# Optimization experiments

Hardware: AMD Instinct MI355X
Metric: run time of the kernel (lower is better)

Reference implementation:

```python
import jax, jax.numpy as jnp
import numpy as np

EPS = 1e-5
HEADS = 4


def _ln(x, s, b):
    m = jnp.mean(x, axis=-1, keepdims=True)
    v = jnp.mean(jnp.square(x - m), axis=-1, keepdims=True)
    return (x - m) * jax.lax.rsqrt(v + EPS) * s + b


def _gru(x, Wg, bg, Wcx, bcx, Wch, bch):
    # In this GRUCell the gates depend only on the inputs, so the gate and
    # candidate_x matmuls are precomputed over all timesteps; only the
    # (reset*h) @ Wch matmul is sequential.
    gx = jax.nn.sigmoid(x @ Wg + bg)   # [B,S,2H]
    cx = x @ Wcx + bcx                 # [B,S,H]
    H = Wch.shape[0]

    def step(h, gc):
        g, c = gc
        r, u = jnp.split(g, 2, axis=-1)
        cand = jnp.tanh(c + (r * h) @ Wch + bch)
        h_new = u * h + (1.0 - u) * cand
        return h_new, h_new

    h0 = jnp.zeros((x.shape[0], H), x.dtype)
    _, ys = jax.lax.scan(step, h0, (gx.transpose(1, 0, 2), cx.transpose(1, 0, 2)))
    return ys.transpose(1, 0, 2)


def _attn(x, s, b, Wq, bq, Wk, bk, Wv, bv, Wo, bo):
    skip = x
    xn = _ln(x, s, b)
    B, S, _ = xn.shape
    QKV = Wq.shape[1]
    hd = QKV // HEADS
    q = (xn @ Wq + bq).reshape(B, S, HEADS, hd)
    k = (xn @ Wk + bk).reshape(B, S, HEADS, hd)
    v = (xn @ Wv + bv).reshape(B, S, HEADS, hd)
    scores = jnp.einsum('bqhd,bkhd->bhqk', q, k) / jnp.sqrt(jnp.asarray(hd, x.dtype))
    probs = jax.nn.softmax(scores, axis=-1)
    o = jnp.einsum('bhqk,bkhd->bqhd', probs, v).reshape(B, S, QKV)
    return o @ Wo + bo + skip


def _forward(x_cgm, x_other, W_in, b_in, ln0_s, ln0_b,
             g0_Wg, g0_bg, g0_Wcx, g0_bcx, g0_Wch, g0_bch, ln1_s, ln1_b,
             g1_Wg, g1_bg, g1_Wcx, g1_bcx, g1_Wch, g1_bch, ln2_s, ln2_b,
             aln_s, aln_b, Wq, bq, Wk, bk, Wv, bv, Wo, bo,
             Wd1, bd1, lnd1_s, lnd1_b, Wd2, bd2, lnd2_s, lnd2_b, Wout, bout):
    # input projection + LN
    x = _ln(x_cgm @ W_in + b_in, ln0_s, ln0_b)
    # GRU block 0 (residual: dims match, 256==256)
    y = _gru(x, g0_Wg, g0_bg, g0_Wcx, g0_bcx, g0_Wch, g0_bch)
    x = _ln(y, ln1_s, ln1_b) + x
    # GRU block 1
    y = _gru(x, g1_Wg, g1_bg, g1_Wcx, g1_bcx, g1_Wch, g1_bch)
    x = _ln(y, ln2_s, ln2_b) + x
    # attention block after every 2nd GRU block
    x = _attn(x, aln_s, aln_b, Wq, bq, Wk, bk, Wv, bv, Wo, bo)
    # pool over time, concat static features, dense head (no residuals: dims differ)
    pooled = jnp.mean(x, axis=1)
    c = jnp.concatenate([pooled, x_other], axis=-1)
    c = _ln(jax.nn.relu(c @ Wd1 + bd1), lnd1_s, lnd1_b)
    c = _ln(jax.nn.relu(c @ Wd2 + bd2), lnd2_s, lnd2_b)
    return (c @ Wout + bout).squeeze(-1)


def setup_inputs() -> dict:
    key = jax.random.key(0)
    ks = iter(jax.random.split(key, 64))

    def nrm(shape, scale=1.0):
        return jax.random.normal(next(ks), shape, jnp.float32) * scale

    B, S, Fc, Fo, D, QKV = 64, 288, 16, 32, 256, 64
    inp = {
        'x_cgm': nrm((B, S, Fc)),
        'x_other': nrm((B, Fo)),
        'W_in': nrm((Fc, D), Fc ** -0.5), 'b_in': jnp.zeros((D,), jnp.float32),
        'ln0_s': jnp.ones((D,), jnp.float32), 'ln0_b': jnp.zeros((D,), jnp.float32),
    }
    for p in ('g0', 'g1'):
        inp[p + '_Wg'] = nrm((D, 2 * D), D ** -0.5)
        inp[p + '_bg'] = jnp.zeros((2 * D,), jnp.float32)
        inp[p + '_Wcx'] = nrm((D, D), D ** -0.5)
        inp[p + '_bcx'] = jnp.zeros((D,), jnp.float32)
        inp[p + '_Wch'] = nrm((D, D), D ** -0.5)
        inp[p + '_bch'] = jnp.zeros((D,), jnp.float32)
    for n in ('ln1', 'ln2', 'aln'):
        inp[n + '_s'] = jnp.ones((D,), jnp.float32)
        inp[n + '_b'] = jnp.zeros((D,), jnp.float32)
    for n in ('Wq', 'Wk', 'Wv'):
        inp[n] = nrm((D, QKV), D ** -0.5)
    for n in ('bq', 'bk', 'bv'):
        inp[n] = jnp.zeros((QKV,), jnp.float32)
    inp['Wo'] = nrm((QKV, D), QKV ** -0.5)
    inp['bo'] = jnp.zeros((D,), jnp.float32)
    inp['Wd1'] = nrm((D + Fo, 128), (D + Fo) ** -0.5)
    inp['bd1'] = jnp.zeros((128,), jnp.float32)
    inp['lnd1_s'] = jnp.ones((128,), jnp.float32)
    inp['lnd1_b'] = jnp.zeros((128,), jnp.float32)
    inp['Wd2'] = nrm((128, 64), 128 ** -0.5)
    inp['bd2'] = jnp.zeros((64,), jnp.float32)
    inp['lnd2_s'] = jnp.ones((64,), jnp.float32)
    inp['lnd2_b'] = jnp.zeros((64,), jnp.float32)
    inp['Wout'] = nrm((64, 1), 64 ** -0.5)
    inp['bout'] = jnp.zeros((1,), jnp.float32)
    return inp


def reference(x_cgm, x_other, W_in, b_in, ln0_s, ln0_b,
              g0_Wg, g0_bg, g0_Wcx, g0_bcx, g0_Wch, g0_bch, ln1_s, ln1_b,
              g1_Wg, g1_bg, g1_Wcx, g1_bcx, g1_Wch, g1_bch, ln2_s, ln2_b,
              aln_s, aln_b, Wq, bq, Wk, bk, Wv, bv, Wo, bo,
              Wd1, bd1, lnd1_s, lnd1_b, Wd2, bd2, lnd2_s, lnd2_b, Wout, bout):
    return _forward(x_cgm, x_other, W_in, b_in, ln0_s, ln0_b,
                    g0_Wg, g0_bg, g0_Wcx, g0_bcx, g0_Wch, g0_bch, ln1_s, ln1_b,
                    g1_Wg, g1_bg, g1_Wcx, g1_bcx, g1_Wch, g1_bch, ln2_s, ln2_b,
                    aln_s, aln_b, Wq, bq, Wk, bk, Wv, bv, Wo, bo,
                    Wd1, bd1, lnd1_s, lnd1_b, Wd2, bd2, lnd2_s, lnd2_b, Wout, bout)
```

## Files before the change

kernel.cpp:

```cpp
#include <hip/hip_runtime.h>
#include <hip/hip_bf16.h>
#include <math.h>


#define EPS 1e-5f
constexpr int B_ = 64, S_ = 288, FC = 16, FO = 32, D_ = 256, QKVN = 64, HD = 16;
constexpr int TOK = B_ * S_;
constexpr int NX = TOK * D_;
constexpr int NG = TOK * 512;

typedef short bf16x8 __attribute__((ext_vector_type(8)));
typedef float f32x4 __attribute__((ext_vector_type(4)));

__device__ __forceinline__ short f2bf(float f) {
  __hip_bfloat16 h = __float2bfloat16(f);
  return __builtin_bit_cast(short, h);
}

__device__ __forceinline__ float blk_sum(float v, float* sc) {
  #pragma unroll
  for (int o = 32; o > 0; o >>= 1) v += __shfl_down(v, o, 64);
  int tid = threadIdx.x;
  int wid = tid >> 6, nw = blockDim.x >> 6;
  __syncthreads();
  if ((tid & 63) == 0) sc[wid] = v;
  __syncthreads();
  float s = 0.f;
  for (int w = 0; w < nw; ++w) s += sc[w];
  return s;
}

__global__ __launch_bounds__(256) void inproj_ln(
    const float* __restrict__ xc, const float* __restrict__ Wi,
    const float* __restrict__ bi, const float* __restrict__ sc_,
    const float* __restrict__ bb, float* __restrict__ X) {
  __shared__ float sc[8];
  int tok = blockIdx.x, j = threadIdx.x;
  const float* xr = xc + tok * FC;
  float acc = bi[j];
  #pragma unroll
  for (int i = 0; i < FC; ++i) acc += xr[i] * Wi[i * D_ + j];
  float m = blk_sum(acc, sc) * (1.f / D_);
  float d = acc - m;
  float var = blk_sum(d * d, sc) * (1.f / D_);
  X[tok * D_ + j] = d * rsqrtf(var + EPS) * sc_[j] + bb[j];
}

template <int RES>
__global__ __launch_bounds__(256) void ln_token(
    const float* __restrict__ in, const float* __restrict__ sc_,
    const float* __restrict__ bb, const float* __restrict__ resid,
    float* __restrict__ out) {
  __shared__ float sc[8];
  int tok = blockIdx.x, j = threadIdx.x;
  float v = in[tok * D_ + j];
  float m = blk_sum(v, sc) * (1.f / D_);
  float d = v - m;
  float var = blk_sum(d * d, sc) * (1.f / D_);
  float r = d * rsqrtf(var + EPS) * sc_[j] + bb[j];
  if (RES) r += resid[tok * D_ + j];
  out[tok * D_ + j] = r;
}

template <int BN, int ACT, int RES>
__global__ __launch_bounds__(256) void gemm_mfma(
    const float* __restrict__ A, const float* __restrict__ W,
    const float* __restrict__ bias, const float* __restrict__ resid,
    float* __restrict__ OUT, int K, int N) {
  constexpr int BM = 128, BK = 32;
  constexpr int NT16 = BN / 16;
  constexpr int BTASK = BN * 4 / 256;
  __shared__ short As[BM * 40];
  __shared__ short Bs[BN * 40];
  int tid = threadIdx.x;
  int wave = tid >> 6, lane = tid & 63;
  int quad = lane >> 4, m16 = lane & 15;
  int row0 = blockIdx.x * BM;
  int bn0 = blockIdx.y * BN;

  f32x4 acc[2][NT16];
  #pragma unroll
  for (int mt = 0; mt < 2; ++mt)
    #pragma unroll
    for (int nt = 0; nt < NT16; ++nt) acc[mt][nt] = (f32x4){0.f, 0.f, 0.f, 0.f};

  const float* Ag = A + (size_t)row0 * K;

  for (int kk = 0; kk < K; kk += BK) {
    __syncthreads();
    #pragma unroll
    for (int i = 0; i < 4; ++i) {
      int t = tid + i * 256;
      int r = t >> 3, kq = t & 7;
      float4 a4 = *(const float4*)(Ag + (size_t)r * K + kk + kq * 4);
      short4 s4 = make_short4(f2bf(a4.x), f2bf(a4.y), f2bf(a4.z), f2bf(a4.w));
      *(short4*)&As[r * 40 + kq * 4] = s4;
    }
    #pragma unroll
    for (int i = 0; i < BTASK; ++i) {
      int t = tid + i * 256;
      int n = t % BN, oct = t / BN;
      const float* bp = W + (size_t)(kk + oct * 8) * N + bn0 + n;
      bf16x8 bv;
      #pragma unroll
      for (int j = 0; j < 8; ++j) bv[j] = f2bf(bp[(size_t)j * N]);
      *(bf16x8*)&Bs[n * 40 + oct * 8] = bv;
    }
    __syncthreads();
    bf16x8 af0 = *(const bf16x8*)&As[(wave * 32 + m16) * 40 + quad * 8];
    bf16x8 af1 = *(const bf16x8*)&As[(wave * 32 + 16 + m16) * 40 + quad * 8];
    #pragma unroll
    for (int nt = 0; nt < NT16; ++nt) {
      bf16x8 bfr = *(const bf16x8*)&Bs[(nt * 16 + m16) * 40 + quad * 8];
      acc[0][nt] = __builtin_amdgcn_mfma_f32_16x16x32_bf16(af0, bfr, acc[0][nt], 0, 0, 0);
      acc[1][nt] = __builtin_amdgcn_mfma_f32_16x16x32_bf16(af1, bfr, acc[1][nt], 0, 0, 0);
    }
  }
  #pragma unroll
  for (int mt = 0; mt < 2; ++mt) {
    #pragma unroll
    for (int nt = 0; nt < NT16; ++nt) {
      int col = bn0 + nt * 16 + m16;
      float bv = bias[col];
      #pragma unroll
      for (int r = 0; r < 4; ++r) {
        int row = row0 + wave * 32 + mt * 16 + quad * 4 + r;
        float v = acc[mt][nt][r] + bv;
        if (ACT == 1) v = 1.f / (1.f + __expf(-v));
        if (RES) v += resid[(size_t)row * N + col];
        OUT[(size_t)row * N + col] = v;
      }
    }
  }
}

__global__ __launch_bounds__(512, 2) void gru_scan(
    const float* __restrict__ G, const float* __restrict__ C,
    const float* __restrict__ Wch, const float* __restrict__ bch,
    float* __restrict__ Y) {
  __shared__ short vstage[2][256];
  int tid = threadIdx.x;
  int b = blockIdx.x;
  int wave = tid >> 6, lane = tid & 63;
  int quad = lane >> 4, m16 = lane & 15;
  int col0 = 32 * wave + m16;
  int col1 = col0 + 16;

  bf16x8 wfrag[2][8];
  #pragma unroll
  for (int tt = 0; tt < 2; ++tt) {
    int n = (tt == 0) ? col0 : col1;
    #pragma unroll
    for (int c = 0; c < 8; ++c) {
      const float* wp = Wch + (size_t)(32 * c + quad * 8) * D_ + n;
      bf16x8 w;
      #pragma unroll
      for (int j = 0; j < 8; ++j) w[j] = f2bf(wp[(size_t)j * D_]);
      wfrag[tt][c] = w;
    }
  }

  const float* Gp = G + (size_t)b * S_ * 512;
  const float* Cp = C + (size_t)b * S_ * 256;
  float* Yp = Y + (size_t)b * S_ * 256;

  float bch0 = bch[col0], bch1 = bch[col1];
  float h0 = 0.f, h1 = 0.f;

  float cu0[4], cu1[4], cc0[4], cc1[4], cr0[4], cr1[4];
  #pragma unroll
  for (int i = 0; i < 4; ++i) {
    cu0[i] = Gp[(size_t)i * 512 + 256 + col0];
    cu1[i] = Gp[(size_t)i * 512 + 256 + col1];
    cc0[i] = Cp[(size_t)i * 256 + col0];
    cc1[i] = Cp[(size_t)i * 256 + col1];
    cr0[i] = Gp[(size_t)(i + 1) * 512 + col0];
    cr1[i] = Gp[(size_t)(i + 1) * 512 + col1];
  }

  if (tid < 256) vstage[0][tid] = 0;
  __syncthreads();

  constexpr int NGRP = S_ / 4;
  for (int g = 0; g < NGRP; ++g) {
    int gn = (g + 1 < NGRP) ? g + 1 : NGRP - 1;
    const float* Gn = Gp + (size_t)gn * 4 * 512;
    const float* Cn = Cp + (size_t)gn * 4 * 256;
    float nu0[4], nu1[4], nc0[4], nc1[4], nr0[4], nr1[4];
    #pragma unroll
    for (int i = 0; i < 4; ++i) {
      nu0[i] = Gn[(size_t)i * 512 + 256 + col0];
      nu1[i] = Gn[(size_t)i * 512 + 256 + col1];
      nc0[i] = Cn[(size_t)i * 256 + col0];
      nc1[i] = Cn[(size_t)i * 256 + col1];
      int ri = (gn * 4 + i + 1 < S_) ? i + 1 : i;
      nr0[i] = Gn[(size_t)ri * 512 + col0];
      nr1[i] = Gn[(size_t)ri * 512 + col1];
    }
    #pragma unroll
    for (int i = 0; i < 4; ++i) {
      int t = g * 4 + i;
      int buf = t & 1;
      f32x4 A0[4], A1[4];
      #pragma unroll
      for (int j = 0; j < 4; ++j) {
        A0[j] = (f32x4){0.f, 0.f, 0.f, 0.f};
        A1[j] = (f32x4){0.f, 0.f, 0.f, 0.f};
      }
      #pragma unroll
      for (int p = 0; p < 2; ++p) {
        #pragma unroll
        for (int j = 0; j < 4; ++j) {
          int c = p * 4 + j;
          bf16x8 af = *(const bf16x8*)&vstage[buf][(c * 4 + quad) * 8];
          A0[j] = __builtin_amdgcn_mfma_f32_16x16x32_bf16(af, wfrag[0][c], A0[j], 0, 0, 0);
          A1[j] = __builtin_amdgcn_mfma_f32_16x16x32_bf16(af, wfrag[1][c], A1[j], 0, 0, 0);
        }
      }
      float s0 = cc0[i] + bch0 + ((A0[0][0] + A0[1][0]) + (A0[2][0] + A0[3][0]));
      float s1 = cc1[i] + bch1 + ((A1[0][0] + A1[1][0]) + (A1[2][0] + A1[3][0]));
      float e0 = __expf(2.f * s0), e1 = __expf(2.f * s1);
      float cand0 = 1.f - 2.f / (e0 + 1.f);
      float cand1 = 1.f - 2.f / (e1 + 1.f);
      h0 = cu0[i] * h0 + (1.f - cu0[i]) * cand0;
      h1 = cu1[i] * h1 + (1.f - cu1[i]) * cand1;
      short v0 = f2bf(cr0[i] * h0), v1 = f2bf(cr1[i] * h1);
      if (quad == 0) {
        Yp[(size_t)t * 256 + col0] = h0;
        Yp[(size_t)t * 256 + col1] = h1;
        vstage[buf ^ 1][col0] = v0;
        vstage[buf ^ 1][col1] = v1;
      }
      __builtin_amdgcn_s_waitcnt(0xC07F);
      __builtin_amdgcn_s_barrier();
    }
    #pragma unroll
    for (int i = 0; i < 4; ++i) {
      cu0[i] = nu0[i]; cu1[i] = nu1[i];
      cc0[i] = nc0[i]; cc1[i] = nc1[i];
      cr0[i] = nr0[i]; cr1[i] = nr1[i];
    }
  }
}

__global__ __launch_bounds__(320) void attn(
    const float* __restrict__ Q, const float* __restrict__ Kv,
    const float* __restrict__ V, float* __restrict__ AO) {
  __shared__ float Kl[S_ * HD];
  __shared__ float Vl[S_ * HD];
  int b = blockIdx.x, hh = blockIdx.y;
  int tid = threadIdx.x;
  int hoff = hh * HD;
  for (int idx = tid; idx < S_ * HD; idx += 320) {
    int row = idx >> 4, d = idx & 15;
    Kl[idx] = Kv[((size_t)(b * S_ + row)) * QKVN + hoff + d];
    Vl[idx] = V[((size_t)(b * S_ + row)) * QKVN + hoff + d];
  }
  __syncthreads();
  if (tid >= S_) return;
  const float* qp = Q + ((size_t)(b * S_ + tid)) * QKVN + hoff;
  float4 q0 = *(const float4*)(qp + 0);
  float4 q1 = *(const float4*)(qp + 4);
  float4 q2 = *(const float4*)(qp + 8);
  float4 q3 = *(const float4*)(qp + 12);
  float m = -1e30f, l = 0.f;
  float4 o0 = {0, 0, 0, 0}, o1 = {0, 0, 0, 0}, o2 = {0, 0, 0, 0},
         o3 = {0, 0, 0, 0};
  for (int k = 0; k < S_; ++k) {
    const float4* kp = (const float4*)&Kl[k * HD];
    float4 k0 = kp[0], k1 = kp[1], k2 = kp[2], k3 = kp[3];
    float s = q0.x * k0.x + q0.y * k0.y + q0.z * k0.z + q0.w * k0.w +
              q1.x * k1.x + q1.y * k1.y + q1.z * k1.z + q1.w * k1.w +
              q2.x * k2.x + q2.y * k2.y + q2.z * k2.z + q2.w * k2.w +
              q3.x * k3.x + q3.y * k3.y + q3.z * k3.z + q3.w * k3.w;
    s *= 0.25f;
    float mn = fmaxf(m, s);
    float corr = __expf(m - mn);
    float p = __expf(s - mn);
    l = l * corr + p;
    const float4* vp = (const float4*)&Vl[k * HD];
    float4 v0 = vp[0], v1 = vp[1], v2 = vp[2], v3 = vp[3];
    o0.x = o0.x * corr + p * v0.x; o0.y = o0.y * corr + p * v0.y;
    o0.z = o0.z * corr + p * v0.z; o0.w = o0.w * corr + p * v0.w;
    o1.x = o1.x * corr + p * v1.x; o1.y = o1.y * corr + p * v1.y;
    o1.z = o1.z * corr + p * v1.z; o1.w = o1.w * corr + p * v1.w;
    o2.x = o2.x * corr + p * v2.x; o2.y = o2.y * corr + p * v2.y;
    o2.z = o2.z * corr + p * v2.z; o2.w = o2.w * corr + p * v2.w;
    o3.x = o3.x * corr + p * v3.x; o3.y = o3.y * corr + p * v3.y;
    o3.z = o3.z * corr + p * v3.z; o3.w = o3.w * corr + p * v3.w;
    m = mn;
  }
  float inv = 1.f / l;
  float* op = AO + ((size_t)(b * S_ + tid)) * QKVN + hoff;
  float4 r0 = {o0.x * inv, o0.y * inv, o0.z * inv, o0.w * inv};
  float4 r1 = {o1.x * inv, o1.y * inv, o1.z * inv, o1.w * inv};
  float4 r2 = {o2.x * inv, o2.y * inv, o2.z * inv, o2.w * inv};
  float4 r3 = {o3.x * inv, o3.y * inv, o3.z * inv, o3.w * inv};
  ((float4*)op)[0] = r0; ((float4*)op)[1] = r1;
  ((float4*)op)[2] = r2; ((float4*)op)[3] = r3;
}

__global__ __launch_bounds__(128) void head(
    const float* __restrict__ X, const float* __restrict__ xo,
    const float* __restrict__ Wd1, const float* __restrict__ bd1,
    const float* __restrict__ s1, const float* __restrict__ b1,
    const float* __restrict__ Wd2, const float* __restrict__ bd2,
    const float* __restrict__ s2, const float* __restrict__ b2,
    const float* __restrict__ Wout, const float* __restrict__ bout,
    float* __restrict__ out) {
  __shared__ float c[D_ + FO];
  __shared__ float h1[128];
  __shared__ float sc[8];
  int b = blockIdx.x, tid = threadIdx.x;
  for (int cc = tid; cc < D_; cc += 128) {
    float acc = 0.f;
    for (int t = 0; t < S_; ++t) acc += X[((size_t)(b * S_ + t)) * D_ + cc];
    c[cc] = acc * (1.f / S_);
  }
  if (tid < FO) c[D_ + tid] = xo[b * FO + tid];
  __syncthreads();
  float v = bd1[tid];
  for (int k = 0; k < D_ + FO; ++k) v += c[k] * Wd1[k * 128 + tid];
  v = fmaxf(v, 0.f);
  float m = blk_sum(v, sc) * (1.f / 128.f);
  float d = v - m;
  float var = blk_sum(d * d, sc) * (1.f / 128.f);
  h1[tid] = d * rsqrtf(var + EPS) * s1[tid] + b1[tid];
  __syncthreads();
  float v2 = 0.f;
  if (tid < 64) {
    v2 = bd2[tid];
    for (int k = 0; k < 128; ++k) v2 += h1[k] * Wd2[k * 64 + tid];
    v2 = fmaxf(v2, 0.f);
  }
  float m2 = blk_sum(tid < 64 ? v2 : 0.f, sc) * (1.f / 64.f);
  float d2v = v2 - m2;
  float var2 = blk_sum(tid < 64 ? d2v * d2v : 0.f, sc) * (1.f / 64.f);
  float hv = (tid < 64) ? (d2v * rsqrtf(var2 + EPS) * s2[tid] + b2[tid]) : 0.f;
  float p = (tid < 64) ? hv * Wout[tid] : 0.f;
  float tot = blk_sum(p, sc);
  if (tid == 0) out[b] = tot + bout[0];
}

extern "C" void kernel_launch(void* const* d_in, const int* in_sizes, int n_in,
                              void* d_out, int out_size, void* d_ws,
                              size_t ws_size, hipStream_t stream) {
  const float* x_cgm = (const float*)d_in[0];
  const float* x_other = (const float*)d_in[1];
  const float* W_in = (const float*)d_in[2];
  const float* b_in = (const float*)d_in[3];
  const float* ln0_s = (const float*)d_in[4];
  const float* ln0_b = (const float*)d_in[5];
  const float* g0_Wg = (const float*)d_in[6];
  const float* g0_bg = (const float*)d_in[7];
  const float* g0_Wcx = (const float*)d_in[8];
  const float* g0_bcx = (const float*)d_in[9];
  const float* g0_Wch = (const float*)d_in[10];
  const float* g0_bch = (const float*)d_in[11];
  const float* g1_Wg = (const float*)d_in[12];
  const float* g1_bg = (const float*)d_in[13];
  const float* g1_Wcx = (const float*)d_in[14];
  const float* g1_bcx = (const float*)d_in[15];
  const float* g1_Wch = (const float*)d_in[16];
  const float* g1_bch = (const float*)d_in[17];
  const float* ln1_s = (const float*)d_in[18];
  const float* ln1_b = (const float*)d_in[19];
  const float* ln2_s = (const float*)d_in[20];
  const float* ln2_b = (const float*)d_in[21];
  const float* aln_s = (const float*)d_in[22];
  const float* aln_b = (const float*)d_in[23];
  const float* Wq = (const float*)d_in[24];
  const float* Wk = (const float*)d_in[25];
  const float* Wv = (const float*)d_in[26];
  const float* bq = (const float*)d_in[27];
  const float* bk = (const float*)d_in[28];
  const float* bv = (const float*)d_in[29];
  const float* Wo = (const float*)d_in[30];
  const float* bo = (const float*)d_in[31];
  const float* Wd1 = (const float*)d_in[32];
  const float* bd1 = (const float*)d_in[33];
  const float* lnd1_s = (const float*)d_in[34];
  const float* lnd1_b = (const float*)d_in[35];
  const float* Wd2 = (const float*)d_in[36];
  const float* bd2 = (const float*)d_in[37];
  const float* lnd2_s = (const float*)d_in[38];
  const float* lnd2_b = (const float*)d_in[39];
  const float* Wout = (const float*)d_in[40];
  const float* bout = (const float*)d_in[41];
  (void)in_sizes; (void)n_in; (void)out_size; (void)ws_size;

  float* ws = (float*)d_ws;
  float* X = ws;
  float* Yb = ws + NX;
  float* Gb = ws + 2 * NX;
  float* Cb = Gb + NG;
  float* Qb = Gb;
  float* Kb = Gb + TOK * QKVN;
  float* Vb = Gb + 2 * TOK * QKVN;
  float* AO = Cb;

  const int MB = TOK / 128;

  inproj_ln<<<TOK, 256, 0, stream>>>(x_cgm, W_in, b_in, ln0_s, ln0_b, X);

  gemm_mfma<128, 1, 0><<<dim3(MB, 4), 256, 0, stream>>>(X, g0_Wg, g0_bg, nullptr, Gb, 256, 512);
  gemm_mfma<128, 0, 0><<<dim3(MB, 2), 256, 0, stream>>>(X, g0_Wcx, g0_bcx, nullptr, Cb, 256, 256);
  gru_scan<<<B_, 512, 0, stream>>>(Gb, Cb, g0_Wch, g0_bch, Yb);
  ln_token<1><<<TOK, 256, 0, stream>>>(Yb, ln1_s, ln1_b, X, X);

  gemm_mfma<128, 1, 0><<<dim3(MB, 4), 256, 0, stream>>>(X, g1_Wg, g1_bg, nullptr, Gb, 256, 512);
  gemm_mfma<128, 0, 0><<<dim3(MB, 2), 256, 0, stream>>>(X, g1_Wcx, g1_bcx, nullptr, Cb, 256, 256);
  gru_scan<<<B_, 512, 0, stream>>>(Gb, Cb, g1_Wch, g1_bch, Yb);
  ln_token<1><<<TOK, 256, 0, stream>>>(Yb, ln2_s, ln2_b, X, X);

  ln_token<0><<<TOK, 256, 0, stream>>>(X, aln_s, aln_b, nullptr, Yb);
  gemm_mfma<64, 0, 0><<<dim3(MB, 1), 256, 0, stream>>>(Yb, Wq, bq, nullptr, Qb, 256, 64);
  gemm_mfma<64, 0, 0><<<dim3(MB, 1), 256, 0, stream>>>(Yb, Wk, bk, nullptr, Kb, 256, 64);
  gemm_mfma<64, 0, 0><<<dim3(MB, 1), 256, 0, stream>>>(Yb, Wv, bv, nullptr, Vb, 256, 64);
  attn<<<dim3(B_, 4), 320, 0, stream>>>(Qb, Kb, Vb, AO);
  gemm_mfma<128, 0, 1><<<dim3(MB, 2), 256, 0, stream>>>(AO, Wo, bo, X, X, 64, 256);

  head<<<B_, 128, 0, stream>>>(X, x_other, Wd1, bd1, lnd1_s, lnd1_b,
                               Wd2, bd2, lnd2_s, lnd2_b, Wout, bout,
                               (float*)d_out);
}
```

Before: 736.6 us.

## Fuse GEMM launches, register-prefetch GEMM K-tiles, merge back-to-back LayerNorms

The gate and candidate GEMMs are merged into one launch, as are the Q/K/V GEMMs. The shared GEMM body now stages K=64 tiles and prefetches the next tile into registers while the MFMAs run on the current one. The post-GRU LayerNorm plus residual is fused with the attention LayerNorm in one kernel, and the head pooling uses 256 threads so each thread owns one column. These changes cut launches and global round trips and overlap loads with compute. In exchange, the GEMMs use more registers and pass act/res as runtime flags instead of template parameters.

```diff
diff --git a/kernel.cpp b/kernel.cpp
--- a/kernel.cpp
+++ b/kernel.cpp
@@ -46,8 +46,7 @@
   X[tok * D_ + j] = d * rsqrtf(var + EPS) * sc_[j] + bb[j];
 }
 
-template <int RES>
-__global__ __launch_bounds__(256) void ln_token(
+__global__ __launch_bounds__(256) void ln_token_res(
     const float* __restrict__ in, const float* __restrict__ sc_,
     const float* __restrict__ bb, const float* __restrict__ resid,
     float* __restrict__ out) {
@@ -57,26 +56,41 @@
   float m = blk_sum(v, sc) * (1.f / D_);
   float d = v - m;
   float var = blk_sum(d * d, sc) * (1.f / D_);
-  float r = d * rsqrtf(var + EPS) * sc_[j] + bb[j];
-  if (RES) r += resid[tok * D_ + j];
-  out[tok * D_ + j] = r;
-}
-
-template <int BN, int ACT, int RES>
-__global__ __launch_bounds__(256) void gemm_mfma(
+  out[tok * D_ + j] = d * rsqrtf(var + EPS) * sc_[j] + bb[j] + resid[tok * D_ + j];
+}
+
+__global__ __launch_bounds__(256) void ln_ln(
+    const float* __restrict__ Y, const float* __restrict__ s2,
+    const float* __restrict__ b2, float* __restrict__ X,
+    const float* __restrict__ sa, const float* __restrict__ ba,
+    float* __restrict__ O) {
+  __shared__ float sc[8];
+  int tok = blockIdx.x, j = threadIdx.x;
+  float v = Y[tok * D_ + j];
+  float m = blk_sum(v, sc) * (1.f / D_);
+  float d = v - m;
+  float var = blk_sum(d * d, sc) * (1.f / D_);
+  float r = d * rsqrtf(var + EPS) * s2[j] + b2[j] + X[tok * D_ + j];
+  X[tok * D_ + j] = r;
+  float m2 = blk_sum(r, sc) * (1.f / D_);
+  float d2 = r - m2;
+  float var2 = blk_sum(d2 * d2, sc) * (1.f / D_);
+  O[tok * D_ + j] = d2 * rsqrtf(var2 + EPS) * sa[j] + ba[j];
+}
+
+template <int BN>
+__device__ __forceinline__ void gemm_body(
     const float* __restrict__ A, const float* __restrict__ W,
     const float* __restrict__ bias, const float* __restrict__ resid,
-    float* __restrict__ OUT, int K, int N) {
-  constexpr int BM = 128, BK = 32;
+    float* __restrict__ OUT, int N, int bn0, int K, int act, int res,
+    short* As, short* Bs) {
+  constexpr int BT = BN * 8 / 256;
   constexpr int NT16 = BN / 16;
-  constexpr int BTASK = BN * 4 / 256;
-  __shared__ short As[BM * 40];
-  __shared__ short Bs[BN * 40];
   int tid = threadIdx.x;
   int wave = tid >> 6, lane = tid & 63;
   int quad = lane >> 4, m16 = lane & 15;
-  int row0 = blockIdx.x * BM;
-  int bn0 = blockIdx.y * BN;
+  int row0 = blockIdx.x * 128;
+  const float* Ag = A + (size_t)row0 * K;
 
   f32x4 acc[2][NT16];
   #pragma unroll
@@ -84,37 +98,73 @@
     #pragma unroll
     for (int nt = 0; nt < NT16; ++nt) acc[mt][nt] = (f32x4){0.f, 0.f, 0.f, 0.f};
 
-  const float* Ag = A + (size_t)row0 * K;
-
-  for (int kk = 0; kk < K; kk += BK) {
-    __syncthreads();
+  float aR[4][8];
+  float bR[BT][8];
+
+  auto loadA = [&](int kk) {
     #pragma unroll
     for (int i = 0; i < 4; ++i) {
-      int t = tid + i * 256;
-      int r = t >> 3, kq = t & 7;
-      float4 a4 = *(const float4*)(Ag + (size_t)r * K + kk + kq * 4);
-      short4 s4 = make_short4(f2bf(a4.x), f2bf(a4.y), f2bf(a4.z), f2bf(a4.w));
-      *(short4*)&As[r * 40 + kq * 4] = s4;
-    }
-    #pragma unroll
-    for (int i = 0; i < BTASK; ++i) {
-      int t = tid + i * 256;
-      int n = t % BN, oct = t / BN;
-      const float* bp = W + (size_t)(kk + oct * 8) * N + bn0 + n;
-      bf16x8 bv;
-      #pragma unroll
-      for (int j = 0; j < 8; ++j) bv[j] = f2bf(bp[(size_t)j * N]);
-      *(bf16x8*)&Bs[n * 40 + oct * 8] = bv;
-    }
-    __syncthreads();
-    bf16x8 af0 = *(const bf16x8*)&As[(wave * 32 + m16) * 40 + quad * 8];
-    bf16x8 af1 = *(const bf16x8*)&As[(wave * 32 + 16 + m16) * 40 + quad * 8];
-    #pragma unroll
-    for (int nt = 0; nt < NT16; ++nt) {
-      bf16x8 bfr = *(const bf16x8*)&Bs[(nt * 16 + m16) * 40 + quad * 8];
-      acc[0][nt] = __builtin_amdgcn_mfma_f32_16x16x32_bf16(af0, bfr, acc[0][nt], 0, 0, 0);
-      acc[1][nt] = __builtin_amdgcn_mfma_f32_16x16x32_bf16(af1, bfr, acc[1][nt], 0, 0, 0);
-    }
+      int idx = tid + i * 256;
+      int r = idx >> 3, oct = idx & 7;
+      const float* p = Ag + (size_t)r * K + kk + oct * 8;
+      float4 x = *(const float4*)p;
+      float4 y = *(const float4*)(p + 4);
+      aR[i][0] = x.x; aR[i][1] = x.y; aR[i][2] = x.z; aR[i][3] = x.w;
+      aR[i][4] = y.x; aR[i][5] = y.y; aR[i][6] = y.z; aR[i][7] = y.w;
+    }
+  };
+  auto loadB = [&](int kk) {
+    #pragma unroll
+    for (int i = 0; i < BT; ++i) {
+      int idx = tid + i * 256;
+      int n = idx & (BN - 1), oct = idx / BN;
+      const float* p = W + (size_t)(kk + oct * 8) * N + bn0 + n;
+      #pragma unroll
+      for (int j = 0; j < 8; ++j) bR[i][j] = p[(size_t)j * N];
+    }
+  };
+  auto storeA = [&]() {
+    #pragma unroll
+    for (int i = 0; i < 4; ++i) {
+      int idx = tid + i * 256;
+      int r = idx >> 3, oct = idx & 7;
+      bf16x8 v;
+      #pragma unroll
+      for (int j = 0; j < 8; ++j) v[j] = f2bf(aR[i][j]);
+      *(bf16x8*)&As[r * 72 + oct * 8] = v;
+    }
+  };
+  auto storeB = [&]() {
+    #pragma unroll
+    for (int i = 0; i < BT; ++i) {
+      int idx = tid + i * 256;
+      int n = idx & (BN - 1), oct = idx / BN;
+      bf16x8 v;
+      #pragma unroll
+      for (int j = 0; j < 8; ++j) v[j] = f2bf(bR[i][j]);
+      *(bf16x8*)&Bs[n * 72 + oct * 8] = v;
+    }
+  };
+
+  loadA(0); loadB(0);
+  for (int kk = 0; kk < K; kk += 64) {
+    storeA(); storeB();
+    __builtin_amdgcn_s_waitcnt(0xC07F);
+    __builtin_amdgcn_s_barrier();
+    if (kk + 64 < K) { loadA(kk + 64); loadB(kk + 64); }
+    #pragma unroll
+    for (int kc = 0; kc < 2; ++kc) {
+      bf16x8 af0 = *(const bf16x8*)&As[(wave * 32 + m16) * 72 + kc * 32 + quad * 8];
+      bf16x8 af1 = *(const bf16x8*)&As[(wave * 32 + 16 + m16) * 72 + kc * 32 + quad * 8];
+      #pragma unroll
+      for (int nt = 0; nt < NT16; ++nt) {
+        bf16x8 bfr = *(const bf16x8*)&Bs[(nt * 16 + m16) * 72 + kc * 32 + quad * 8];
+        acc[0][nt] = __builtin_amdgcn_mfma_f32_16x16x32_bf16(af0, bfr, acc[0][nt], 0, 0, 0);
+        acc[1][nt] = __builtin_amdgcn_mfma_f32_16x16x32_bf16(af1, bfr, acc[1][nt], 0, 0, 0);
+      }
+    }
+    __builtin_amdgcn_s_waitcnt(0xC07F);
+    __builtin_amdgcn_s_barrier();
   }
   #pragma unroll
   for (int mt = 0; mt < 2; ++mt) {
@@ -126,12 +176,49 @@
       for (int r = 0; r < 4; ++r) {
         int row = row0 + wave * 32 + mt * 16 + quad * 4 + r;
         float v = acc[mt][nt][r] + bv;
-        if (ACT == 1) v = 1.f / (1.f + __expf(-v));
-        if (RES) v += resid[(size_t)row * N + col];
+        if (act) v = 1.f / (1.f + __expf(-v));
+        if (res) v += resid[(size_t)row * N + col];
         OUT[(size_t)row * N + col] = v;
       }
     }
   }
+}
+
+__global__ __launch_bounds__(256) void gemm_gru(
+    const float* __restrict__ A, const float* __restrict__ Wg,
+    const float* __restrict__ bg, const float* __restrict__ Wc,
+    const float* __restrict__ bc, float* __restrict__ G,
+    float* __restrict__ Cc) {
+  __shared__ short As[128 * 72];
+  __shared__ short Bs[128 * 72];
+  bool isG = blockIdx.y < 4;
+  gemm_body<128>(A, isG ? Wg : Wc, isG ? bg : bc, nullptr, isG ? G : Cc,
+                 isG ? 512 : 256, (isG ? blockIdx.y : blockIdx.y - 4) * 128,
+                 256, isG ? 1 : 0, 0, As, Bs);
+}
+
+__global__ __launch_bounds__(256) void gemm_qkv(
+    const float* __restrict__ A, const float* __restrict__ Wq,
+    const float* __restrict__ bq, const float* __restrict__ Wk,
+    const float* __restrict__ bk, const float* __restrict__ Wv,
+    const float* __restrict__ bv, float* __restrict__ Q,
+    float* __restrict__ Kb, float* __restrict__ V) {
+  __shared__ short As[128 * 72];
+  __shared__ short Bs[64 * 72];
+  int y = blockIdx.y;
+  const float* W = (y == 0) ? Wq : (y == 1) ? Wk : Wv;
+  const float* bi = (y == 0) ? bq : (y == 1) ? bk : bv;
+  float* O = (y == 0) ? Q : (y == 1) ? Kb : V;
+  gemm_body<64>(A, W, bi, nullptr, O, 64, 0, 256, 0, 0, As, Bs);
+}
+
+__global__ __launch_bounds__(256) void gemm_proj(
+    const float* __restrict__ A, const float* __restrict__ W,
+    const float* __restrict__ bi, const float* __restrict__ resid,
+    float* __restrict__ O) {
+  __shared__ short As[128 * 72];
+  __shared__ short Bs[128 * 72];
+  gemm_body<128>(A, W, bi, resid, O, 256, blockIdx.y * 128, 64, 0, 1, As, Bs);
 }
 
 __global__ __launch_bounds__(512, 2) void gru_scan(
@@ -300,7 +387,7 @@
   ((float4*)op)[2] = r2; ((float4*)op)[3] = r3;
 }
 
-__global__ __launch_bounds__(128) void head(
+__global__ __launch_bounds__(256) void head(
     const float* __restrict__ X, const float* __restrict__ xo,
     const float* __restrict__ Wd1, const float* __restrict__ bd1,
     const float* __restrict__ s1, const float* __restrict__ b1,
@@ -312,20 +399,25 @@
   __shared__ float h1[128];
   __shared__ float sc[8];
   int b = blockIdx.x, tid = threadIdx.x;
-  for (int cc = tid; cc < D_; cc += 128) {
+  {
     float acc = 0.f;
-    for (int t = 0; t < S_; ++t) acc += X[((size_t)(b * S_ + t)) * D_ + cc];
-    c[cc] = acc * (1.f / S_);
+    const float* xp = X + (size_t)b * S_ * D_ + tid;
+    #pragma unroll 4
+    for (int t = 0; t < S_; ++t) acc += xp[(size_t)t * D_];
+    c[tid] = acc * (1.f / S_);
   }
   if (tid < FO) c[D_ + tid] = xo[b * FO + tid];
   __syncthreads();
-  float v = bd1[tid];
-  for (int k = 0; k < D_ + FO; ++k) v += c[k] * Wd1[k * 128 + tid];
-  v = fmaxf(v, 0.f);
-  float m = blk_sum(v, sc) * (1.f / 128.f);
+  float v = 0.f;
+  if (tid < 128) {
+    v = bd1[tid];
+    for (int k = 0; k < D_ + FO; ++k) v += c[k] * Wd1[k * 128 + tid];
+    v = fmaxf(v, 0.f);
+  }
+  float m = blk_sum(tid < 128 ? v : 0.f, sc) * (1.f / 128.f);
   float d = v - m;
-  float var = blk_sum(d * d, sc) * (1.f / 128.f);
-  h1[tid] = d * rsqrtf(var + EPS) * s1[tid] + b1[tid];
+  float var = blk_sum(tid < 128 ? d * d : 0.f, sc) * (1.f / 128.f);
+  if (tid < 128) h1[tid] = d * rsqrtf(var + EPS) * s1[tid] + b1[tid];
   __syncthreads();
   float v2 = 0.f;
   if (tid < 64) {
@@ -403,24 +495,20 @@
 
   inproj_ln<<<TOK, 256, 0, stream>>>(x_cgm, W_in, b_in, ln0_s, ln0_b, X);
 
-  gemm_mfma<128, 1, 0><<<dim3(MB, 4), 256, 0, stream>>>(X, g0_Wg, g0_bg, nullptr, Gb, 256, 512);
-  gemm_mfma<128, 0, 0><<<dim3(MB, 2), 256, 0, stream>>>(X, g0_Wcx, g0_bcx, nullptr, Cb, 256, 256);
+  gemm_gru<<<dim3(MB, 6), 256, 0, stream>>>(X, g0_Wg, g0_bg, g0_Wcx, g0_bcx, Gb, Cb);
   gru_scan<<<B_, 512, 0, stream>>>(Gb, Cb, g0_Wch, g0_bch, Yb);
-  ln_token<1><<<TOK, 256, 0, stream>>>(Yb, ln1_s, ln1_b, X, X);
-
-  gemm_mfma<128, 1, 0><<<dim3(MB, 4), 256, 0, stream>>>(X, g1_Wg, g1_bg, nullptr, Gb, 256, 512);
-  gemm_mfma<128, 0, 0><<<dim3(MB, 2), 256, 0, stream>>>(X, g1_Wcx, g1_bcx, nullptr, Cb, 256, 256);
+  ln_token_res<<<TOK, 256, 0, stream>>>(Yb, ln1_s, ln1_b, X, X);
+
+  gemm_gru<<<dim3(MB, 6), 256, 0, stream>>>(X, g1_Wg, g1_bg, g1_Wcx, g1_bcx, Gb, Cb);
   gru_scan<<<B_, 512, 0, stream>>>(Gb, Cb, g1_Wch, g1_bch, Yb);
-  ln_token<1><<<TOK, 256, 0, stream>>>(Yb, ln2_s, ln2_b, X, X);
-
-  ln_token<0><<<TOK, 256, 0, stream>>>(X, aln_s, aln_b, nullptr, Yb);
-  gemm_mfma<64, 0, 0><<<dim3(MB, 1), 256, 0, stream>>>(Yb, Wq, bq, nullptr, Qb, 256, 64);
-  gemm_mfma<64, 0, 0><<<dim3(MB, 1), 256, 0, stream>>>(Yb, Wk, bk, nullptr, Kb, 256, 64);
-  gemm_mfma<64, 0, 0><<<dim3(MB, 1), 256, 0, stream>>>(Yb, Wv, bv, nullptr, Vb, 256, 64);
+
+  ln_ln<<<TOK, 256, 0, stream>>>(Yb, ln2_s, ln2_b, X, aln_s, aln_b, Yb);
+
+  gemm_qkv<<<dim3(MB, 3), 256, 0, stream>>>(Yb, Wq, bq, Wk, bk, Wv, bv, Qb, Kb, Vb);
   attn<<<dim3(B_, 4), 320, 0, stream>>>(Qb, Kb, Vb, AO);
-  gemm_mfma<128, 0, 1><<<dim3(MB, 2), 256, 0, stream>>>(AO, Wo, bo, X, X, 64, 256);
-
-  head<<<B_, 128, 0, stream>>>(X, x_other, Wd1, bd1, lnd1_s, lnd1_b,
+  gemm_proj<<<dim3(MB, 2), 256, 0, stream>>>(AO, Wo, bo, X, X);
+
+  head<<<B_, 256, 0, stream>>>(X, x_other, Wd1, bd1, lnd1_s, lnd1_b,
                                Wd2, bd2, lnd2_s, lnd2_b, Wout, bout,
                                (float*)d_out);
 }
```

Result: faster. 702.3 us (-4.7%).
